# Optimization experiments

Hardware: AMD Instinct MI355X
Metric: run time of the kernel (lower is better)

Reference implementation:

```python
import jax, jax.numpy as jnp
import numpy as np


def setup_inputs() -> dict:
    key0 = jax.random.key(0)
    k1, k2, k3, k4 = jax.random.split(key0, 4)
    bs, h, S, dk = 4, 16, 2048, 64
    query = jax.random.normal(k1, (bs * h, S, dk), dtype=jnp.float32)
    key = jax.random.normal(k2, (bs * h, S, dk), dtype=jnp.float32)
    value = jax.random.normal(k3, (bs * h, S, dk), dtype=jnp.float32)
    attn_mask = jax.random.randint(k4, (bs, S), 0, 2, dtype=jnp.int64)
    return {"query": query, "key": key, "value": value, "attn_mask": attn_mask}


def reference(query, key, value, attn_mask):
    bs_h, K, dk = key.shape
    Q = query.shape[1]
    bs = attn_mask.shape[0]
    h = bs_h // bs
    # [bs_h, Q, K] scores, scaled by sqrt(d_k)
    scores = jnp.einsum('bqd,bkd->bqk', query, key) / jnp.sqrt(jnp.asarray(dk, query.dtype))
    # mask==0 positions get an additive -1e-10 (faithful to original, incl. its tiny magnitude)
    m = (attn_mask == 0).astype(scores.dtype)          # [bs, K]
    m = jnp.tile(m, (h, 1))[:, None, :]                # [bs_h, 1, K] (torch .repeat(h,1) tiles)
    scores = scores + m * (-1e-10)
    attn = jax.nn.softmax(scores, axis=-1)
    # dropout p=0.0 (identity in this deterministic reference)
    return jnp.einsum('bqk,bkd->bqd', attn, value)
```

## Files before the change

### kernel.cpp

```cpp
#include <hip/hip_runtime.h>
#include <hip/hip_bf16.h>
#include <stdint.h>

typedef __bf16 bf16x8 __attribute__((ext_vector_type(8)));
typedef float  f32x4  __attribute__((ext_vector_type(4)));
typedef float  f32x16 __attribute__((ext_vector_type(16)));
typedef int    i32x2  __attribute__((ext_vector_type(2)));
typedef unsigned short u16x8 __attribute__((ext_vector_type(8)));

#define S_LEN 2048
#define DK    64
#define KVBLK 64
#define NT    (S_LEN / KVBLK)
#define QW    32
#define QBLK  128
#define TILE_E (KVBLK * DK)

static __device__ __forceinline__ unsigned short f2bf(float f) {
    union { float f; unsigned u; } v; v.f = f;
    unsigned r = v.u + 0x7fffu + ((v.u >> 16) & 1u);
    return (unsigned short)(r >> 16);
}

static __device__ __forceinline__ float fexp2(float x) {
#if __has_builtin(__builtin_amdgcn_exp2f)
    return __builtin_amdgcn_exp2f(x);
#else
    return exp2f(x);
#endif
}

static __device__ __forceinline__ unsigned cvtpk(float lo, float hi) {
    unsigned r;
    asm("v_cvt_pk_bf16_f32 %0, %1, %2" : "=v"(r) : "v"(lo), "v"(hi));
    return r;
}

static __device__ __forceinline__ i32x2 plswap(int a, int b) {
#if __has_builtin(__builtin_amdgcn_permlane32_swap)
    return __builtin_amdgcn_permlane32_swap(a, b, false, false);
#else
    const bool up = (threadIdx.x & 32) != 0;
    int as = __shfl_xor(a, 32, 64);
    int bs = __shfl_xor(b, 32, 64);
    i32x2 r;
    r[0] = up ? bs : a;
    r[1] = up ? b  : as;
    return r;
#endif
}
static __device__ __forceinline__ float xhalf_sum(float x) {
    union { float f; int i; } u; u.f = x;
    i32x2 t = plswap(u.i, u.i);
    union { int i; float f; } a, b; a.i = t[0]; b.i = t[1];
    return a.f + b.f;
}

__global__ __launch_bounds__(256)
void conv_all(const float* __restrict__ Q, const float* __restrict__ K,
              const float* __restrict__ V,
              unsigned short* __restrict__ Qb, unsigned short* __restrict__ Kb,
              unsigned short* __restrict__ Vb, int tiles) {
    __shared__ unsigned short tile[KVBLK][DK + 2];
    const int b = blockIdx.x;
    const int tid = threadIdx.x;
    if (b < tiles) {
        const float* src = K + (size_t)b * TILE_E;
        unsigned short* dst = Kb + (size_t)b * TILE_E;
        #pragma unroll
        for (int g = 0; g < 2; ++g) {
            const int p   = tid * 8 + g * 2048;
            const int f   = p >> 8;
            const int ln  = (p >> 3) & 31;
            const int sub = f >> 3, ds = (f >> 1) & 3, hi = f & 1;
            const float* s = src + (sub * 32 + ln) * DK + ds * 16 + hi * 8;
            u16x8 o;
            #pragma unroll
            for (int j = 0; j < 8; ++j) o[j] = f2bf(s[j]);
            *(u16x8*)&dst[p] = o;
        }
    } else if (b < 2 * tiles) {
        const int bb = b - tiles;
        const float* src = V + (size_t)bb * TILE_E;
        const int k = tid >> 2, c = (tid & 3) * 16;
        #pragma unroll
        for (int j = 0; j < 16; ++j) tile[k][c + j] = f2bf(src[k * DK + c + j]);
        __syncthreads();
        unsigned short* dst = Vb + (size_t)bb * TILE_E;
        #pragma unroll
        for (int g = 0; g < 2; ++g) {
            const int p    = tid * 8 + g * 2048;
            const int g2   = p >> 8;
            const int ln   = (p >> 3) & 31;
            const int hi   = g2 & 1, dblk = (g2 >> 1) & 1, ks = (g2 >> 2) & 1, sub = g2 >> 3;
            const int k0   = sub * 32 + ks * 16 + hi * 8;
            const int d    = dblk * 32 + ln;
            u16x8 o;
            #pragma unroll
            for (int j = 0; j < 8; ++j) o[j] = tile[k0 + j][d];
            *(u16x8*)&dst[p] = o;
        }
    } else {
        const size_t i = ((size_t)(b - 2 * tiles) * 256 + tid) * 8;
        const float4 v0 = *(const float4*)(Q + i);
        const float4 v1 = *(const float4*)(Q + i + 4);
        const float s = 0.125f * 1.44269504089f;
        u16x8 o;
        o[0] = f2bf(v0.x * s); o[1] = f2bf(v0.y * s);
        o[2] = f2bf(v0.z * s); o[3] = f2bf(v0.w * s);
        o[4] = f2bf(v1.x * s); o[5] = f2bf(v1.y * s);
        o[6] = f2bf(v1.z * s); o[7] = f2bf(v1.w * s);
        *(u16x8*)&Qb[i] = o;
    }
}


__global__ __launch_bounds__(256)
void sdpa_fwd2(const unsigned short* __restrict__ Qb,
               const unsigned short* __restrict__ Kb,
               const unsigned short* __restrict__ Vb,
               float* __restrict__ O) {
    __shared__ __align__(16) char smem[32768];

    const int tid  = threadIdx.x;
    const int lane = tid & 63;
    const int wave = tid >> 6;
    const int ln   = lane & 31;
    const int hi   = lane >> 5;

    const int head = blockIdx.y;
    const int q0   = blockIdx.x * QBLK + wave * QW;

    const unsigned short* KbH = Kb + (size_t)head * NT * TILE_E;
    const unsigned short* VbH = Vb + (size_t)head * NT * TILE_E;

    u16x8 qfrag[4];
    {
        const unsigned short* qsrc = Qb + ((size_t)head * S_LEN + q0 + ln) * DK + hi * 8;
        #pragma unroll
        for (int ds = 0; ds < 4; ++ds) qfrag[ds] = *(const u16x8*)&qsrc[ds * 16];
    }

    auto STAGE = [&](int t, int b) {
        const unsigned short* Kt = KbH + (size_t)t * TILE_E;
        const unsigned short* Vt = VbH + (size_t)t * TILE_E;
        unsigned short* sKb = (unsigned short*)(smem + b * 16384);
        unsigned short* sVb = (unsigned short*)(smem + b * 16384 + 8192);
        #pragma unroll
        for (int i = 0; i < 2; ++i) {
            __builtin_amdgcn_global_load_lds(
                (const __attribute__((address_space(1))) void*)(Kt + i * 2048 + tid * 8),
                (__attribute__((address_space(3))) void*)(&sKb[i * 2048 + wave * 512]),
                16, 0, 0);
            __builtin_amdgcn_global_load_lds(
                (const __attribute__((address_space(1))) void*)(Vt + i * 2048 + tid * 8),
                (__attribute__((address_space(3))) void*)(&sVb[i * 2048 + wave * 512]),
                16, 0, 0);
        }
    };

    f32x16 oacc[2];
    #pragma unroll
    for (int dblk = 0; dblk < 2; ++dblk)
        #pragma unroll
        for (int r = 0; r < 16; ++r) oacc[dblk][r] = 0.0f;
    float lsum = 0.0f;

    const int lbase = hi * 512 + ln * 16;

    STAGE(0, 0);

    #pragma unroll 2
    for (int t = 0; t < NT; ++t) {
        const int cur = t & 1;
        if (t + 1 < NT) {
            STAGE(t + 1, cur ^ 1);
            asm volatile("s_waitcnt vmcnt(4)" ::: "memory");
        } else {
            asm volatile("s_waitcnt vmcnt(0)" ::: "memory");
        }
        __builtin_amdgcn_s_barrier();
        __builtin_amdgcn_sched_barrier(0);

        const char* sK  = (const char*)(smem + cur * 16384) + lbase;
        const char* sVT = (const char*)(smem + cur * 16384 + 8192) + lbase;

        f32x16 sacc[2];
        #pragma unroll
        for (int sub = 0; sub < 2; ++sub)
            #pragma unroll
            for (int r = 0; r < 16; ++r) sacc[sub][r] = 0.0f;
        __builtin_amdgcn_s_setprio(1);
        #pragma unroll
        for (int sub = 0; sub < 2; ++sub) {
            #pragma unroll
            for (int ds = 0; ds < 4; ++ds) {
                u16x8 kf = *(const u16x8*)(sK + sub * 4096 + ds * 1024);
                sacc[sub] = __builtin_amdgcn_mfma_f32_32x32x16_bf16(
                    __builtin_bit_cast(bf16x8, kf), __builtin_bit_cast(bf16x8, qfrag[ds]),
                    sacc[sub], 0, 0, 0);
            }
        }
        __builtin_amdgcn_s_setprio(0);

        float s0 = 0.f, s1 = 0.f, s2 = 0.f, s3 = 0.f;
        #pragma unroll
        for (int sub = 0; sub < 2; ++sub)
            #pragma unroll
            for (int i = 0; i < 16; i += 4) {
                float e0 = fexp2(sacc[sub][i]);
                float e1 = fexp2(sacc[sub][i + 1]);
                float e2 = fexp2(sacc[sub][i + 2]);
                float e3 = fexp2(sacc[sub][i + 3]);
                sacc[sub][i] = e0; sacc[sub][i + 1] = e1;
                sacc[sub][i + 2] = e2; sacc[sub][i + 3] = e3;
                s0 += e0; s1 += e1; s2 += e2; s3 += e3;
            }
        lsum += (s0 + s1) + (s2 + s3);

        u16x8 pa[2][2];
        #pragma unroll
        for (int sub = 0; sub < 2; ++sub) {
            unsigned w[8];
            #pragma unroll
            for (int i = 0; i < 8; ++i)
                w[i] = cvtpk(sacc[sub][2 * i], sacc[sub][2 * i + 1]);
            i32x2 a0 = plswap((int)w[0], (int)w[2]);
            i32x2 a1 = plswap((int)w[1], (int)w[3]);
            i32x2 a2 = plswap((int)w[4], (int)w[6]);
            i32x2 a3 = plswap((int)w[5], (int)w[7]);
            unsigned pk0[4] = { (unsigned)a0[0], (unsigned)a1[0], (unsigned)a0[1], (unsigned)a1[1] };
            unsigned pk1[4] = { (unsigned)a2[0], (unsigned)a3[0], (unsigned)a2[1], (unsigned)a3[1] };
            pa[sub][0] = *(u16x8*)pk0;
            pa[sub][1] = *(u16x8*)pk1;
        }

        __builtin_amdgcn_s_setprio(1);
        #pragma unroll
        for (int sub = 0; sub < 2; ++sub)
            #pragma unroll
            for (int dblk = 0; dblk < 2; ++dblk) {
                #pragma unroll
                for (int ks = 0; ks < 2; ++ks) {
                    u16x8 vf = *(const u16x8*)(sVT + sub * 4096 + ks * 2048 + dblk * 1024);
                    oacc[dblk] = __builtin_amdgcn_mfma_f32_32x32x16_bf16(
                        __builtin_bit_cast(bf16x8, vf), __builtin_bit_cast(bf16x8, pa[sub][ks]),
                        oacc[dblk], 0, 0, 0);
                }
            }
        __builtin_amdgcn_s_setprio(0);

        __builtin_amdgcn_s_barrier();
    }

    const float inv = 1.0f / xhalf_sum(lsum);

    float* tp = (float*)(smem + wave * 8192);
    __syncthreads();
    #pragma unroll
    for (int dblk = 0; dblk < 2; ++dblk)
        #pragma unroll
        for (int r = 0; r < 16; ++r) {
            const int d = dblk * 32 + (r & 3) + 8 * (r >> 2) + 4 * hi;
            tp[d * 32 + ln] = oacc[dblk][r] * inv;
        }
    __syncthreads();
    {
        const int qloc = lane >> 1;
        const int dh   = (lane & 1) * 32;
        float* Orow = O + ((size_t)head * S_LEN + q0 + qloc) * DK + dh;
        #pragma unroll
        for (int c = 0; c < 8; ++c) {
            float4 v;
            v.x = tp[(dh + c * 4 + 0) * 32 + qloc];
            v.y = tp[(dh + c * 4 + 1) * 32 + qloc];
            v.z = tp[(dh + c * 4 + 2) * 32 + qloc];
            v.w = tp[(dh + c * 4 + 3) * 32 + qloc];
            *(float4*)(Orow + c * 4) = v;
        }
    }
}


__global__ __launch_bounds__(256)
void sdpa_fwd_fb(const float* __restrict__ Q, const float* __restrict__ K,
                 const float* __restrict__ V, float* __restrict__ O) {
    __shared__ unsigned short sK[KVBLK * DK];
    __shared__ unsigned short sVT[DK * KVBLK];
    __shared__ unsigned short sP[4][16 * KVBLK];
    const int tid = threadIdx.x, lane = tid & 63, wave = tid >> 6;
    const int lo = lane & 15, hi = lane >> 4;
    const int head = blockIdx.y;
    const int q0 = blockIdx.x * 64 + wave * 16;
    const float* Qh = Q + (size_t)head * S_LEN * DK;
    const float* Kh = K + (size_t)head * S_LEN * DK;
    const float* Vh = V + (size_t)head * S_LEN * DK;
    bf16x8 qfrag[2];
    {
        const int qrow = q0 + lo;
        for (int ks = 0; ks < 2; ++ks) {
            const float* p = Qh + (size_t)qrow * DK + ks * 32 + hi * 8;
            u16x8 u;
            #pragma unroll
            for (int j = 0; j < 8; ++j) u[j] = f2bf(p[j] * 0.125f);
            qfrag[ks] = __builtin_bit_cast(bf16x8, u);
        }
    }
    f32x4 oacc[4];
    #pragma unroll
    for (int dc = 0; dc < 4; ++dc) for (int i = 0; i < 4; ++i) oacc[dc][i] = 0.0f;
    float mrow[4] = {-1e30f, -1e30f, -1e30f, -1e30f};
    float lrow[4] = {0.f, 0.f, 0.f, 0.f};
    for (int kv = 0; kv < S_LEN; kv += KVBLK) {
        {
            const int k = tid >> 2, c = tid & 3;
            const float* src = Kh + (size_t)(kv + k) * DK + c * 16;
            u16x8 a, b;
            #pragma unroll
            for (int j = 0; j < 8; ++j) a[j] = f2bf(src[j]);
            #pragma unroll
            for (int j = 0; j < 8; ++j) b[j] = f2bf(src[8 + j]);
            const int sw = (k & 7) << 3, base = k * DK + c * 16;
            *(u16x8*)&sK[(base) ^ sw] = a;
            *(u16x8*)&sK[(base + 8) ^ sw] = b;
        }
        {
            const int d = tid & 63, sw = (d & 7) << 3;
            #pragma unroll
            for (int half = 0; half < 2; ++half) {
                const int k0 = (tid >> 6) * 8 + half * 32;
                u16x8 v;
                #pragma unroll
                for (int j = 0; j < 8; ++j) v[j] = f2bf(Vh[(size_t)(kv + k0 + j) * DK + d]);
                *(u16x8*)&sVT[(d * KVBLK + k0) ^ sw] = v;
            }
        }
        __syncthreads();
        f32x4 sacc[4];
        #pragma unroll
        for (int kc = 0; kc < 4; ++kc) for (int i = 0; i < 4; ++i) sacc[kc][i] = 0.0f;
        #pragma unroll
        for (int kc = 0; kc < 4; ++kc) {
            const int krow = kc * 16 + lo, sw = (krow & 7) << 3;
            #pragma unroll
            for (int ks = 0; ks < 2; ++ks) {
                u16x8 u = *(const u16x8*)&sK[(krow * DK + ks * 32 + hi * 8) ^ sw];
                sacc[kc] = __builtin_amdgcn_mfma_f32_16x16x32_bf16(
                    qfrag[ks], __builtin_bit_cast(bf16x8, u), sacc[kc], 0, 0, 0);
            }
        }
        float pv[4][4], mnew[4], sc[4];
        #pragma unroll
        for (int r = 0; r < 4; ++r) {
            float t = fmaxf(fmaxf(sacc[0][r], sacc[1][r]), fmaxf(sacc[2][r], sacc[3][r]));
            #pragma unroll
            for (int mm = 1; mm <= 8; mm <<= 1) t = fmaxf(t, __shfl_xor(t, mm, 64));
            mnew[r] = fmaxf(mrow[r], t);
            sc[r] = __expf(mrow[r] - mnew[r]);
        }
        #pragma unroll
        for (int r = 0; r < 4; ++r) {
            float s = 0.f;
            #pragma unroll
            for (int kc = 0; kc < 4; ++kc) { float e = __expf(sacc[kc][r] - mnew[r]); pv[kc][r] = e; s += e; }
            #pragma unroll
            for (int mm = 1; mm <= 8; mm <<= 1) s += __shfl_xor(s, mm, 64);
            lrow[r] = lrow[r] * sc[r] + s;
            mrow[r] = mnew[r];
        }
        #pragma unroll
        for (int dc = 0; dc < 4; ++dc)
            #pragma unroll
            for (int r = 0; r < 4; ++r) oacc[dc][r] *= sc[r];
        unsigned short* sPw = sP[wave];
        #pragma unroll
        for (int r = 0; r < 4; ++r) {
            const int row = hi * 4 + r, sw = (row & 7) << 3;
            #pragma unroll
            for (int kc = 0; kc < 4; ++kc)
                sPw[(row * KVBLK + kc * 16 + lo) ^ sw] = f2bf(pv[kc][r]);
        }
        bf16x8 pfrag[2];
        {
            const int sw = (lo & 7) << 3;
            #pragma unroll
            for (int ks = 0; ks < 2; ++ks) {
                u16x8 u = *(const u16x8*)&sPw[(lo * KVBLK + ks * 32 + hi * 8) ^ sw];
                pfrag[ks] = __builtin_bit_cast(bf16x8, u);
            }
        }
        #pragma unroll
        for (int dc = 0; dc < 4; ++dc) {
            const int d = dc * 16 + lo, sw = (d & 7) << 3;
            #pragma unroll
            for (int ks = 0; ks < 2; ++ks) {
                u16x8 u = *(const u16x8*)&sVT[(d * KVBLK + ks * 32 + hi * 8) ^ sw];
                oacc[dc] = __builtin_amdgcn_mfma_f32_16x16x32_bf16(
                    pfrag[ks], __builtin_bit_cast(bf16x8, u), oacc[dc], 0, 0, 0);
            }
        }
        __syncthreads();
    }
    float* Oh = O + (size_t)head * S_LEN * DK;
    #pragma unroll
    for (int r = 0; r < 4; ++r) {
        const float inv = 1.0f / lrow[r];
        const int row = q0 + hi * 4 + r;
        #pragma unroll
        for (int dc = 0; dc < 4; ++dc)
            Oh[(size_t)row * DK + dc * 16 + lo] = oacc[dc][r] * inv;
    }
}

extern "C" void kernel_launch(void* const* d_in, const int* in_sizes, int n_in,
                              void* d_out, int out_size, void* d_ws, size_t ws_size,
                              hipStream_t stream) {
    const float* Q = (const float*)d_in[0];
    const float* K = (const float*)d_in[1];
    const float* V = (const float*)d_in[2];
    float* O = (float*)d_out;
    const int heads = in_sizes[0] / (S_LEN * DK);
    const size_t n  = (size_t)heads * S_LEN * DK;
    const size_t need = 3 * n * sizeof(unsigned short);

    if (ws_size >= need) {
        unsigned short* Qb = (unsigned short*)d_ws;
        unsigned short* Kb = Qb + n;
        unsigned short* Vb = Kb + n;
        const int tiles = (int)(n / TILE_E);
        const int qblocks = (int)(n / 8 / 256);
        conv_all<<<2 * tiles + qblocks, 256, 0, stream>>>(Q, K, V, Qb, Kb, Vb, tiles);
        dim3 grid(S_LEN / QBLK, heads);
        sdpa_fwd2<<<grid, 256, 0, stream>>>(Qb, Kb, Vb, O);
    } else {
        dim3 grid(S_LEN / 64, heads);
        sdpa_fwd_fb<<<grid, 256, 0, stream>>>(Q, K, V, O);
    }
}
```

Baseline: 114.8 us.

## Triple-buffer KV tiles, software-pipeline QK with PV, and remap blocks per XCD

New measurement: 110.3 us. -3.9%, faster.

```diff
diff --git a/kernel.cpp b/kernel.cpp
--- a/kernel.cpp
+++ b/kernel.cpp
@@ -120,7 +120,7 @@
                const unsigned short* __restrict__ Kb,
                const unsigned short* __restrict__ Vb,
                float* __restrict__ O) {
-    __shared__ __align__(16) char smem[32768];
+    __shared__ __align__(16) char smem[49152];
 
     const int tid  = threadIdx.x;
     const int lane = tid & 63;
@@ -128,8 +128,12 @@
     const int ln   = lane & 31;
     const int hi   = lane >> 5;
 
-    const int head = blockIdx.y;
-    const int q0   = blockIdx.x * QBLK + wave * QW;
+    const int flat = blockIdx.x;
+    const int xcd  = flat & 7;
+    const int rr   = flat >> 3;
+    const int qb_i = rr & 15;
+    const int head = (rr >> 4) * 8 + xcd;
+    const int q0   = qb_i * QBLK + wave * QW;
 
     const unsigned short* KbH = Kb + (size_t)head * NT * TILE_E;
     const unsigned short* VbH = Vb + (size_t)head * NT * TILE_E;
@@ -159,6 +163,27 @@
         }
     };
 
+    const int lbase = hi * 512 + ln * 16;
+
+    auto QK = [&](int b, f32x16* s) {
+        const char* sK = (const char*)smem + b * 16384 + lbase;
+        #pragma unroll
+        for (int sub = 0; sub < 2; ++sub)
+            #pragma unroll
+            for (int r = 0; r < 16; ++r) s[sub][r] = 0.0f;
+        __builtin_amdgcn_s_setprio(1);
+        #pragma unroll
+        for (int sub = 0; sub < 2; ++sub)
+            #pragma unroll
+            for (int ds = 0; ds < 4; ++ds) {
+                u16x8 kf = *(const u16x8*)(sK + sub * 4096 + ds * 1024);
+                s[sub] = __builtin_amdgcn_mfma_f32_32x32x16_bf16(
+                    __builtin_bit_cast(bf16x8, kf), __builtin_bit_cast(bf16x8, qfrag[ds]),
+                    s[sub], 0, 0, 0);
+            }
+        __builtin_amdgcn_s_setprio(0);
+    };
+
     f32x16 oacc[2];
     #pragma unroll
     for (int dblk = 0; dblk < 2; ++dblk)
@@ -166,65 +191,28 @@
         for (int r = 0; r < 16; ++r) oacc[dblk][r] = 0.0f;
     float lsum = 0.0f;
 
-    const int lbase = hi * 512 + ln * 16;
-
-    STAGE(0, 0);
-
-    #pragma unroll 2
-    for (int t = 0; t < NT; ++t) {
-        const int cur = t & 1;
-        if (t + 1 < NT) {
-            STAGE(t + 1, cur ^ 1);
-            asm volatile("s_waitcnt vmcnt(4)" ::: "memory");
-        } else {
-            asm volatile("s_waitcnt vmcnt(0)" ::: "memory");
-        }
-        __builtin_amdgcn_s_barrier();
-        __builtin_amdgcn_sched_barrier(0);
-
-        const char* sK  = (const char*)(smem + cur * 16384) + lbase;
-        const char* sVT = (const char*)(smem + cur * 16384 + 8192) + lbase;
-
-        f32x16 sacc[2];
+    u16x8 pa[2][2];
+    auto SMPACK = [&](f32x16* s) {
+        float s0 = 0.f, s1 = 0.f, s2 = 0.f, s3 = 0.f;
         #pragma unroll
         for (int sub = 0; sub < 2; ++sub)
             #pragma unroll
-            for (int r = 0; r < 16; ++r) sacc[sub][r] = 0.0f;
-        __builtin_amdgcn_s_setprio(1);
-        #pragma unroll
-        for (int sub = 0; sub < 2; ++sub) {
-            #pragma unroll
-            for (int ds = 0; ds < 4; ++ds) {
-                u16x8 kf = *(const u16x8*)(sK + sub * 4096 + ds * 1024);
-                sacc[sub] = __builtin_amdgcn_mfma_f32_32x32x16_bf16(
-                    __builtin_bit_cast(bf16x8, kf), __builtin_bit_cast(bf16x8, qfrag[ds]),
-                    sacc[sub], 0, 0, 0);
-            }
-        }
-        __builtin_amdgcn_s_setprio(0);
-
-        float s0 = 0.f, s1 = 0.f, s2 = 0.f, s3 = 0.f;
-        #pragma unroll
-        for (int sub = 0; sub < 2; ++sub)
-            #pragma unroll
             for (int i = 0; i < 16; i += 4) {
-                float e0 = fexp2(sacc[sub][i]);
-                float e1 = fexp2(sacc[sub][i + 1]);
-                float e2 = fexp2(sacc[sub][i + 2]);
-                float e3 = fexp2(sacc[sub][i + 3]);
-                sacc[sub][i] = e0; sacc[sub][i + 1] = e1;
-                sacc[sub][i + 2] = e2; sacc[sub][i + 3] = e3;
+                float e0 = fexp2(s[sub][i]);
+                float e1 = fexp2(s[sub][i + 1]);
+                float e2 = fexp2(s[sub][i + 2]);
+                float e3 = fexp2(s[sub][i + 3]);
+                s[sub][i] = e0; s[sub][i + 1] = e1;
+                s[sub][i + 2] = e2; s[sub][i + 3] = e3;
                 s0 += e0; s1 += e1; s2 += e2; s3 += e3;
             }
         lsum += (s0 + s1) + (s2 + s3);
-
-        u16x8 pa[2][2];
         #pragma unroll
         for (int sub = 0; sub < 2; ++sub) {
             unsigned w[8];
             #pragma unroll
             for (int i = 0; i < 8; ++i)
-                w[i] = cvtpk(sacc[sub][2 * i], sacc[sub][2 * i + 1]);
+                w[i] = cvtpk(s[sub][2 * i], s[sub][2 * i + 1]);
             i32x2 a0 = plswap((int)w[0], (int)w[2]);
             i32x2 a1 = plswap((int)w[1], (int)w[3]);
             i32x2 a2 = plswap((int)w[4], (int)w[6]);
@@ -234,12 +222,14 @@
             pa[sub][0] = *(u16x8*)pk0;
             pa[sub][1] = *(u16x8*)pk1;
         }
-
+    };
+    auto PV = [&](int b) {
+        const char* sVT = (const char*)smem + b * 16384 + 8192 + lbase;
         __builtin_amdgcn_s_setprio(1);
         #pragma unroll
         for (int sub = 0; sub < 2; ++sub)
             #pragma unroll
-            for (int dblk = 0; dblk < 2; ++dblk) {
+            for (int dblk = 0; dblk < 2; ++dblk)
                 #pragma unroll
                 for (int ks = 0; ks < 2; ++ks) {
                     u16x8 vf = *(const u16x8*)(sVT + sub * 4096 + ks * 2048 + dblk * 1024);
@@ -247,14 +237,43 @@
                         __builtin_bit_cast(bf16x8, vf), __builtin_bit_cast(bf16x8, pa[sub][ks]),
                         oacc[dblk], 0, 0, 0);
                 }
-            }
         __builtin_amdgcn_s_setprio(0);
-
+    };
+
+    STAGE(0, 0);
+    asm volatile("s_waitcnt vmcnt(0)" ::: "memory");
+    __builtin_amdgcn_s_barrier();
+    STAGE(1, 1);
+    f32x16 S[2], Snext[2];
+    QK(0, S);
+
+    int bPV = 0, bQK = 1, bST = 2;
+
+    for (int t = 0; t < NT - 2; ++t) {
+        asm volatile("s_waitcnt vmcnt(0)" ::: "memory");
         __builtin_amdgcn_s_barrier();
-    }
+        STAGE(t + 2, bST);
+        SMPACK(S);
+        QK(bQK, Snext);
+        PV(bPV);
+        #pragma unroll
+        for (int sub = 0; sub < 2; ++sub) Snext[sub] = S[sub] = Snext[sub];
+        S[0] = Snext[0]; S[1] = Snext[1];
+        const int tmp = bPV; bPV = bQK; bQK = bST; bST = tmp;
+    }
+
+    asm volatile("s_waitcnt vmcnt(0)" ::: "memory");
+    __builtin_amdgcn_s_barrier();
+    SMPACK(S);
+    QK(bQK, Snext);
+    PV(bPV);
+    S[0] = Snext[0]; S[1] = Snext[1];
+    { const int tmp = bPV; bPV = bQK; bQK = bST; bST = tmp; }
+
+    SMPACK(S);
+    PV(bPV);
 
     const float inv = 1.0f / xhalf_sum(lsum);
-
     float* tp = (float*)(smem + wave * 8192);
     __syncthreads();
     #pragma unroll
@@ -430,8 +449,7 @@
         const int tiles = (int)(n / TILE_E);
         const int qblocks = (int)(n / 8 / 256);
         conv_all<<<2 * tiles + qblocks, 256, 0, stream>>>(Q, K, V, Qb, Kb, Vb, tiles);
-        dim3 grid(S_LEN / QBLK, heads);
-        sdpa_fwd2<<<grid, 256, 0, stream>>>(Qb, Kb, Vb, O);
+        sdpa_fwd2<<<heads * (S_LEN / QBLK), 256, 0, stream>>>(Qb, Kb, Vb, O);
     } else {
         dim3 grid(S_LEN / 64, heads);
         sdpa_fwd_fb<<<grid, 256, 0, stream>>>(Q, K, V, O);
```

## Process 64 queries per wave, triple-buffer KV tiles, remap blocks per XCD

Applied to the files above, without the earlier changes.

Result: faster. 107.3 us (-6.5%).

```diff
diff --git a/kernel.cpp b/kernel.cpp
--- a/kernel.cpp
+++ b/kernel.cpp
@@ -12,8 +12,9 @@
 #define DK    64
 #define KVBLK 64
 #define NT    (S_LEN / KVBLK)
-#define QW    32
-#define QBLK  128
+#define QW    64
+#define NWAVE 4
+#define QBLK  (QW * NWAVE)
 #define TILE_E (KVBLK * DK)
 
 static __device__ __forceinline__ unsigned short f2bf(float f) {
@@ -120,7 +121,7 @@
                const unsigned short* __restrict__ Kb,
                const unsigned short* __restrict__ Vb,
                float* __restrict__ O) {
-    __shared__ __align__(16) char smem[32768];
+    __shared__ __align__(16) char smem[49152];
 
     const int tid  = threadIdx.x;
     const int lane = tid & 63;
@@ -128,17 +129,23 @@
     const int ln   = lane & 31;
     const int hi   = lane >> 5;
 
-    const int head = blockIdx.y;
-    const int q0   = blockIdx.x * QBLK + wave * QW;
+    const int flat = blockIdx.x;
+    const int xcd  = flat & 7;
+    const int rr   = flat >> 3;
+    const int qb_i = rr & 7;
+    const int head = (rr >> 3) * 8 + xcd;
+    const int q0w  = qb_i * QBLK + wave * QW;
 
     const unsigned short* KbH = Kb + (size_t)head * NT * TILE_E;
     const unsigned short* VbH = Vb + (size_t)head * NT * TILE_E;
 
-    u16x8 qfrag[4];
-    {
-        const unsigned short* qsrc = Qb + ((size_t)head * S_LEN + q0 + ln) * DK + hi * 8;
-        #pragma unroll
-        for (int ds = 0; ds < 4; ++ds) qfrag[ds] = *(const u16x8*)&qsrc[ds * 16];
+    u16x8 qfrag[2][4];
+    #pragma unroll
+    for (int qb = 0; qb < 2; ++qb) {
+        const unsigned short* qsrc =
+            Qb + ((size_t)head * S_LEN + q0w + qb * 32 + ln) * DK + hi * 8;
+        #pragma unroll
+        for (int ds = 0; ds < 4; ++ds) qfrag[qb][ds] = *(const u16x8*)&qsrc[ds * 16];
     }
 
     auto STAGE = [&](int t, int b) {
@@ -159,116 +166,137 @@
         }
     };
 
-    f32x16 oacc[2];
+    const int lbase = hi * 512 + ln * 16;
+
+    f32x16 oacc[2][2];
     #pragma unroll
-    for (int dblk = 0; dblk < 2; ++dblk)
-        #pragma unroll
-        for (int r = 0; r < 16; ++r) oacc[dblk][r] = 0.0f;
-    float lsum = 0.0f;
-
-    const int lbase = hi * 512 + ln * 16;
+    for (int qb = 0; qb < 2; ++qb)
+        #pragma unroll
+        for (int dblk = 0; dblk < 2; ++dblk)
+            #pragma unroll
+            for (int r = 0; r < 16; ++r) oacc[qb][dblk][r] = 0.0f;
+    float lsum0 = 0.0f, lsum1 = 0.0f;
+
+    auto COMPUTE = [&](int b) {
+        const char* base = (const char*)smem + b * 16384;
+        #pragma unroll
+        for (int sub = 0; sub < 2; ++sub) {
+            f32x16 S0, S1;
+            #pragma unroll
+            for (int r = 0; r < 16; ++r) { S0[r] = 0.0f; S1[r] = 0.0f; }
+            const char* sK = base + sub * 4096 + lbase;
+            __builtin_amdgcn_s_setprio(1);
+            #pragma unroll
+            for (int ds = 0; ds < 4; ++ds) {
+                u16x8 kf = *(const u16x8*)(sK + ds * 1024);
+                S0 = __builtin_amdgcn_mfma_f32_32x32x16_bf16(
+                    __builtin_bit_cast(bf16x8, kf), __builtin_bit_cast(bf16x8, qfrag[0][ds]),
+                    S0, 0, 0, 0);
+                S1 = __builtin_amdgcn_mfma_f32_32x32x16_bf16(
+                    __builtin_bit_cast(bf16x8, kf), __builtin_bit_cast(bf16x8, qfrag[1][ds]),
+                    S1, 0, 0, 0);
+            }
+            __builtin_amdgcn_s_setprio(0);
+
+            u16x8 pa0[2], pa1[2];
+            {
+                float a0 = 0.f, a1 = 0.f, a2 = 0.f, a3 = 0.f;
+                #pragma unroll
+                for (int i = 0; i < 16; i += 4) {
+                    float e0 = fexp2(S0[i]);     float e1 = fexp2(S0[i + 1]);
+                    float e2 = fexp2(S0[i + 2]); float e3 = fexp2(S0[i + 3]);
+                    S0[i] = e0; S0[i + 1] = e1; S0[i + 2] = e2; S0[i + 3] = e3;
+                    a0 += e0; a1 += e1; a2 += e2; a3 += e3;
+                }
+                lsum0 += (a0 + a1) + (a2 + a3);
+                unsigned w[8];
+                #pragma unroll
+                for (int i = 0; i < 8; ++i) w[i] = cvtpk(S0[2 * i], S0[2 * i + 1]);
+                i32x2 b0 = plswap((int)w[0], (int)w[2]);
+                i32x2 b1 = plswap((int)w[1], (int)w[3]);
+                i32x2 b2 = plswap((int)w[4], (int)w[6]);
+                i32x2 b3 = plswap((int)w[5], (int)w[7]);
+                unsigned pk0[4] = { (unsigned)b0[0], (unsigned)b1[0], (unsigned)b0[1], (unsigned)b1[1] };
+                unsigned pk1[4] = { (unsigned)b2[0], (unsigned)b3[0], (unsigned)b2[1], (unsigned)b3[1] };
+                pa0[0] = *(u16x8*)pk0;
+                pa0[1] = *(u16x8*)pk1;
+            }
+            {
+                float a0 = 0.f, a1 = 0.f, a2 = 0.f, a3 = 0.f;
+                #pragma unroll
+                for (int i = 0; i < 16; i += 4) {
+                    float e0 = fexp2(S1[i]);     float e1 = fexp2(S1[i + 1]);
+                    float e2 = fexp2(S1[i + 2]); float e3 = fexp2(S1[i + 3]);
+                    S1[i] = e0; S1[i + 1] = e1; S1[i + 2] = e2; S1[i + 3] = e3;
+                    a0 += e0; a1 += e1; a2 += e2; a3 += e3;
+                }
+                lsum1 += (a0 + a1) + (a2 + a3);
+                unsigned w[8];
+                #pragma unroll
+                for (int i = 0; i < 8; ++i) w[i] = cvtpk(S1[2 * i], S1[2 * i + 1]);
+                i32x2 b0 = plswap((int)w[0], (int)w[2]);
+                i32x2 b1 = plswap((int)w[1], (int)w[3]);
+                i32x2 b2 = plswap((int)w[4], (int)w[6]);
+                i32x2 b3 = plswap((int)w[5], (int)w[7]);
+                unsigned pk0[4] = { (unsigned)b0[0], (unsigned)b1[0], (unsigned)b0[1], (unsigned)b1[1] };
+                unsigned pk1[4] = { (unsigned)b2[0], (unsigned)b3[0], (unsigned)b2[1], (unsigned)b3[1] };
+                pa1[0] = *(u16x8*)pk0;
+                pa1[1] = *(u16x8*)pk1;
+            }
+
+            const char* sVT = base + 8192 + sub * 4096 + lbase;
+            __builtin_amdgcn_s_setprio(1);
+            #pragma unroll
+            for (int dblk = 0; dblk < 2; ++dblk)
+                #pragma unroll
+                for (int ks = 0; ks < 2; ++ks) {
+                    u16x8 vf = *(const u16x8*)(sVT + ks * 2048 + dblk * 1024);
+                    oacc[0][dblk] = __builtin_amdgcn_mfma_f32_32x32x16_bf16(
+                        __builtin_bit_cast(bf16x8, vf), __builtin_bit_cast(bf16x8, pa0[ks]),
+                        oacc[0][dblk], 0, 0, 0);
+                    oacc[1][dblk] = __builtin_amdgcn_mfma_f32_32x32x16_bf16(
+                        __builtin_bit_cast(bf16x8, vf), __builtin_bit_cast(bf16x8, pa1[ks]),
+                        oacc[1][dblk], 0, 0, 0);
+                }
+            __builtin_amdgcn_s_setprio(0);
+        }
+    };
 
     STAGE(0, 0);
-
-    #pragma unroll 2
+    STAGE(1, 1);
+    asm volatile("s_waitcnt vmcnt(4)" ::: "memory");
+    __builtin_amdgcn_s_barrier();
+
+    int bC = 0, bN = 1, bS = 2;
     for (int t = 0; t < NT; ++t) {
-        const int cur = t & 1;
-        if (t + 1 < NT) {
-            STAGE(t + 1, cur ^ 1);
-            asm volatile("s_waitcnt vmcnt(4)" ::: "memory");
-        } else {
+        if (t > 0) {
             asm volatile("s_waitcnt vmcnt(0)" ::: "memory");
-        }
-        __builtin_amdgcn_s_barrier();
-        __builtin_amdgcn_sched_barrier(0);
-
-        const char* sK  = (const char*)(smem + cur * 16384) + lbase;
-        const char* sVT = (const char*)(smem + cur * 16384 + 8192) + lbase;
-
-        f32x16 sacc[2];
-        #pragma unroll
-        for (int sub = 0; sub < 2; ++sub)
-            #pragma unroll
-            for (int r = 0; r < 16; ++r) sacc[sub][r] = 0.0f;
-        __builtin_amdgcn_s_setprio(1);
-        #pragma unroll
-        for (int sub = 0; sub < 2; ++sub) {
-            #pragma unroll
-            for (int ds = 0; ds < 4; ++ds) {
-                u16x8 kf = *(const u16x8*)(sK + sub * 4096 + ds * 1024);
-                sacc[sub] = __builtin_amdgcn_mfma_f32_32x32x16_bf16(
-                    __builtin_bit_cast(bf16x8, kf), __builtin_bit_cast(bf16x8, qfrag[ds]),
-                    sacc[sub], 0, 0, 0);
-            }
-        }
-        __builtin_amdgcn_s_setprio(0);
-
-        float s0 = 0.f, s1 = 0.f, s2 = 0.f, s3 = 0.f;
-        #pragma unroll
-        for (int sub = 0; sub < 2; ++sub)
-            #pragma unroll
-            for (int i = 0; i < 16; i += 4) {
-                float e0 = fexp2(sacc[sub][i]);
-                float e1 = fexp2(sacc[sub][i + 1]);
-                float e2 = fexp2(sacc[sub][i + 2]);
-                float e3 = fexp2(sacc[sub][i + 3]);
-                sacc[sub][i] = e0; sacc[sub][i + 1] = e1;
-                sacc[sub][i + 2] = e2; sacc[sub][i + 3] = e3;
-                s0 += e0; s1 += e1; s2 += e2; s3 += e3;
-            }
-        lsum += (s0 + s1) + (s2 + s3);
-
-        u16x8 pa[2][2];
-        #pragma unroll
-        for (int sub = 0; sub < 2; ++sub) {
-            unsigned w[8];
-            #pragma unroll
-            for (int i = 0; i < 8; ++i)
-                w[i] = cvtpk(sacc[sub][2 * i], sacc[sub][2 * i + 1]);
-            i32x2 a0 = plswap((int)w[0], (int)w[2]);
-            i32x2 a1 = plswap((int)w[1], (int)w[3]);
-            i32x2 a2 = plswap((int)w[4], (int)w[6]);
-            i32x2 a3 = plswap((int)w[5], (int)w[7]);
-            unsigned pk0[4] = { (unsigned)a0[0], (unsigned)a1[0], (unsigned)a0[1], (unsigned)a1[1] };
-            unsigned pk1[4] = { (unsigned)a2[0], (unsigned)a3[0], (unsigned)a2[1], (unsigned)a3[1] };
-            pa[sub][0] = *(u16x8*)pk0;
-            pa[sub][1] = *(u16x8*)pk1;
-        }
-
-        __builtin_amdgcn_s_setprio(1);
-        #pragma unroll
-        for (int sub = 0; sub < 2; ++sub)
-            #pragma unroll
-            for (int dblk = 0; dblk < 2; ++dblk) {
-                #pragma unroll
-                for (int ks = 0; ks < 2; ++ks) {
-                    u16x8 vf = *(const u16x8*)(sVT + sub * 4096 + ks * 2048 + dblk * 1024);
-                    oacc[dblk] = __builtin_amdgcn_mfma_f32_32x32x16_bf16(
-                        __builtin_bit_cast(bf16x8, vf), __builtin_bit_cast(bf16x8, pa[sub][ks]),
-                        oacc[dblk], 0, 0, 0);
-                }
-            }
-        __builtin_amdgcn_s_setprio(0);
-
-        __builtin_amdgcn_s_barrier();
-    }
-
-    const float inv = 1.0f / xhalf_sum(lsum);
+            __builtin_amdgcn_s_barrier();
+        }
+        if (t + 2 < NT) STAGE(t + 2, bS);
+        COMPUTE(bC);
+        const int tmp = bC; bC = bN; bN = bS; bS = tmp;
+    }
+
+    const float inv0 = 1.0f / xhalf_sum(lsum0);
+    const float inv1 = 1.0f / xhalf_sum(lsum1);
 
     float* tp = (float*)(smem + wave * 8192);
-    __syncthreads();
     #pragma unroll
-    for (int dblk = 0; dblk < 2; ++dblk)
-        #pragma unroll
-        for (int r = 0; r < 16; ++r) {
-            const int d = dblk * 32 + (r & 3) + 8 * (r >> 2) + 4 * hi;
-            tp[d * 32 + ln] = oacc[dblk][r] * inv;
-        }
-    __syncthreads();
-    {
+    for (int qb = 0; qb < 2; ++qb) {
+        const float inv = qb ? inv1 : inv0;
+        __syncthreads();
+        #pragma unroll
+        for (int dblk = 0; dblk < 2; ++dblk)
+            #pragma unroll
+            for (int r = 0; r < 16; ++r) {
+                const int d = dblk * 32 + (r & 3) + 8 * (r >> 2) + 4 * hi;
+                tp[d * 32 + ln] = oacc[qb][dblk][r] * inv;
+            }
+        __syncthreads();
         const int qloc = lane >> 1;
         const int dh   = (lane & 1) * 32;
-        float* Orow = O + ((size_t)head * S_LEN + q0 + qloc) * DK + dh;
+        float* Orow = O + ((size_t)head * S_LEN + q0w + qb * 32 + qloc) * DK + dh;
         #pragma unroll
         for (int c = 0; c < 8; ++c) {
             float4 v;
@@ -430,8 +458,7 @@
         const int tiles = (int)(n / TILE_E);
         const int qblocks = (int)(n / 8 / 256);
         conv_all<<<2 * tiles + qblocks, 256, 0, stream>>>(Q, K, V, Qb, Kb, Vb, tiles);
-        dim3 grid(S_LEN / QBLK, heads);
-        sdpa_fwd2<<<grid, 256, 0, stream>>>(Qb, Kb, Vb, O);
+        sdpa_fwd2<<<heads * (S_LEN / QBLK), 256, 0, stream>>>(Qb, Kb, Vb, O);
     } else {
         dim3 grid(S_LEN / 64, heads);
         sdpa_fwd_fb<<<grid, 256, 0, stream>>>(Q, K, V, O);
```
